# Optimization experiments

Measured on AMD Instinct MI355X. Metric: run time of the kernel, lower is better.

The kernel has to match this reference:

```python
import jax, jax.numpy as jnp
import numpy as np

N = 100000      # nodes
E = 3200000     # edges (avg degree 32)
IN_CH = 32
EDGE_DIM = 11
HID = IN_CH + 4 + EDGE_DIM   # 47
OUT = 128


def setup_inputs() -> dict:
    key = jax.random.key(0)
    ks = jax.random.split(key, 10)
    x = jax.random.normal(ks[0], (N, IN_CH), dtype=jnp.float32)
    pos = jax.random.normal(ks[1], (N, 3), dtype=jnp.float32) * 10.0
    nrm = jax.random.normal(ks[2], (N, 3), dtype=jnp.float32)
    normal = nrm / jnp.linalg.norm(nrm, axis=1, keepdims=True)
    # edges with src != dst (avoids degenerate zero-distance point pairs)
    src = jax.random.randint(ks[3], (E,), 0, N)
    off = jax.random.randint(ks[4], (E,), 1, N)
    dst = (src + off) % N
    edge_index = jnp.stack([src, dst], axis=0).astype(jnp.int64)
    edge_attr = jax.random.normal(ks[5], (E, EDGE_DIM), dtype=jnp.float32)
    W1 = jax.random.normal(ks[6], (HID, HID), dtype=jnp.float32) / np.sqrt(HID)
    b1 = jnp.zeros((HID,), dtype=jnp.float32)
    g1 = jnp.ones((HID,), dtype=jnp.float32)
    be1 = jnp.zeros((HID,), dtype=jnp.float32)
    W2 = jax.random.normal(ks[7], (HID, OUT), dtype=jnp.float32) / np.sqrt(HID)
    b2 = jnp.zeros((OUT,), dtype=jnp.float32)
    g2 = jnp.ones((OUT,), dtype=jnp.float32)
    be2 = jnp.zeros((OUT,), dtype=jnp.float32)
    return {"x": x, "pos": pos, "normal": normal, "edge_attr": edge_attr,
            "W1": W1, "b1": b1, "g1": g1, "be1": be1,
            "W2": W2, "b2": b2, "g2": g2, "be2": be2,
            "edge_index": edge_index}


def _angle(v1, v2):
    return jnp.arctan2(jnp.linalg.norm(jnp.cross(v1, v2), axis=1),
                       jnp.sum(v1 * v2, axis=1))


def _layernorm(h, g, b, eps=1e-5):
    mu = jnp.mean(h, axis=-1, keepdims=True)
    var = jnp.var(h, axis=-1, keepdims=True)  # biased, matches torch LayerNorm
    return (h - mu) / jnp.sqrt(var + eps) * g + b


def reference(x, pos, normal, edge_attr, W1, b1, g1, be1, W2, b2, g2, be2, edge_index):
    src, dst = edge_index[0], edge_index[1]  # message flows src(j) -> dst(i)
    pos_i, pos_j = pos[dst], pos[src]
    n_i, n_j = normal[dst], normal[src]
    x_j = x[src]
    pseudo = pos_j - pos_i                                  # [E,3]
    ppf = jnp.stack([jnp.linalg.norm(pseudo, axis=1),
                     _angle(n_i, pseudo),
                     _angle(n_j, pseudo),
                     _angle(n_i, n_j)], axis=1)             # [E,4]
    msg = jnp.concatenate([x_j, ppf, edge_attr], axis=1)    # [E,47]
    # local_nn = MLP([47,47,128]): (Lin->ReLU->LayerNorm->Dropout(eval)) x2
    h = _layernorm(jax.nn.relu(msg @ W1 + b1), g1, be1)     # [E,47]
    h = _layernorm(jax.nn.relu(h @ W2 + b2), g2, be2)       # [E,128]
    out = jax.ops.segment_max(h, dst, num_segments=N)       # scatter-max per target node
    return jnp.where(jnp.isfinite(out), out, 0.0)           # nodes w/o edges -> 0
```

## Files before the change

kernel.cpp:

```cpp
#include <hip/hip_runtime.h>
#include <cstdint>
#include <cstddef>


typedef _Float16 f16x8 __attribute__((ext_vector_type(8)));
typedef _Float16 f16x2 __attribute__((ext_vector_type(2)));
typedef float    f32x4 __attribute__((ext_vector_type(4)));

#define ENC_NEGINF 0x007FFFFFu
#define LDK 64
#define LDH 132

__device__ __forceinline__ int swz(int row, int col) {
    return (col & 7) | ((((col >> 3) ^ row) & 7) << 3);
}

__device__ __forceinline__ unsigned fenc(float f) {
    unsigned u = __float_as_uint(f);
    return (u & 0x80000000u) ? ~u : (u | 0x80000000u);
}

__device__ __forceinline__ float fdec(unsigned k) {
    if (k == ENC_NEGINF) return 0.0f;
    unsigned u = (k & 0x80000000u) ? (k ^ 0x80000000u) : ~k;
    return __uint_as_float(u);
}

__device__ __forceinline__ f16x2 pkrtz(float a, float b) {
    auto p = __builtin_amdgcn_cvt_pkrtz(a, b);
    return __builtin_bit_cast(f16x2, p);
}

__global__ void init_out_kernel(unsigned* __restrict__ out, int n4) {
    int i = blockIdx.x * blockDim.x + threadIdx.x;
    if (i < n4)
        ((uint4*)out)[i] = make_uint4(ENC_NEGINF, ENC_NEGINF, ENC_NEGINF, ENC_NEGINF);
}

__global__ void finalize_out_kernel(float* __restrict__ out, int n4) {
    int i = blockIdx.x * blockDim.x + threadIdx.x;
    if (i < n4) {
        uint4 k = ((const uint4*)out)[i];
        float4 r;
        r.x = fdec(k.x); r.y = fdec(k.y); r.z = fdec(k.z); r.w = fdec(k.w);
        ((float4*)out)[i] = r;
    }
}

__global__ void zero_kernel(int* __restrict__ p, int n) {
    int i = blockIdx.x * blockDim.x + threadIdx.x;
    if (i < n) p[i] = 0;
}

__global__ void hist_kernel(const int* __restrict__ dstI, int* __restrict__ counts, int E) {
    int i = blockIdx.x * blockDim.x + threadIdx.x;
    if (i < E) atomicAdd(&counts[dstI[i]], 1);
}

__global__ __launch_bounds__(1024) void scan_blk(const int* __restrict__ in,
                                                 int* __restrict__ outp,
                                                 int* __restrict__ bsums, int N) {
    __shared__ int wsum[16];
    const int tid = threadIdx.x, lane = tid & 63, wid = tid >> 6;
    int i = blockIdx.x * 1024 + tid;
    int v = (i < N) ? in[i] : 0;
    int incl = v;
#pragma unroll
    for (int m = 1; m < 64; m <<= 1) {
        int t = __shfl_up(incl, m, 64);
        if (lane >= m) incl += t;
    }
    if (lane == 63) wsum[wid] = incl;
    __syncthreads();
    int woff = 0;
#pragma unroll
    for (int k = 0; k < 16; ++k) woff += (k < wid) ? wsum[k] : 0;
    if (i < N) outp[i] = woff + incl - v;
    if (tid == 1023 && bsums != nullptr) bsums[blockIdx.x] = woff + incl;
}

__global__ void scatter_kernel(const int* __restrict__ srcI, const int* __restrict__ dstI,
                               int* __restrict__ nextp, const int* __restrict__ bsums,
                               int2* __restrict__ se, int* __restrict__ dst_g, int E) {
    int i = blockIdx.x * blockDim.x + threadIdx.x;
    if (i < E) {
        int d = dstI[i];
        int p = bsums[d >> 10] + atomicAdd(&nextp[d], 1);
        se[p] = make_int2(srcI[i], i);
        dst_g[p] = d;
    }
}

__global__ __launch_bounds__(512, 4) void edge_kernel_csr(
    const float* __restrict__ x,   const float* __restrict__ pos,
    const float* __restrict__ nrm, const float* __restrict__ ea,
    const float* __restrict__ W1,  const float* __restrict__ b1,
    const float* __restrict__ g1,  const float* __restrict__ be1,
    const float* __restrict__ W2,  const float* __restrict__ b2,
    const float* __restrict__ g2,  const float* __restrict__ be2,
    const int2* __restrict__ se,   const int* __restrict__ dst_g,
    unsigned* __restrict__ out, int E, int ntiles, int tilesPerBlock)
{
    __shared__ _Float16 W1t[48][LDK];
    __shared__ _Float16 W2t[128][LDK];
    __shared__ _Float16 msgA[128][LDK];
    __shared__ _Float16 h2w[128][LDH];
    __shared__ int dstL[128];

    const int lane = threadIdx.x & 63;
    const int w    = threadIdx.x >> 6;
    const int c16  = lane & 15;
    const int g    = lane >> 4;
    const int row0 = w * 16;

    for (int i = threadIdx.x; i < 48 * 64; i += 512) {
        int n = i >> 6, k = i & 63;
        W1t[n][swz(n, k)] = (n < 47 && k < 47) ? (_Float16)W1[k * 47 + n] : (_Float16)0.f;
    }
    for (int i = threadIdx.x; i < 128 * 64; i += 512) {
        int n = i >> 6, k = i & 63;
        W2t[n][swz(n, k)] = (k < 47) ? (_Float16)W2[k * 128 + n] : (_Float16)0.f;
    }
    for (int i = threadIdx.x; i < 128 * LDK; i += 512)
        (&msgA[0][0])[i] = (_Float16)0.f;

    float b1v[3], g1v[3], be1v[3];
#pragma unroll
    for (int n = 0; n < 3; ++n) {
        int cc = n * 16 + c16;
        bool vld = cc < 47;
        b1v[n]  = vld ? b1[cc]  : 0.f;
        g1v[n]  = vld ? g1[cc]  : 0.f;
        be1v[n] = vld ? be1[cc] : 0.f;
    }
    float b2v[8];
    f16x2 g2pk[4], be2pk[4];
#pragma unroll
    for (int n = 0; n < 8; ++n) b2v[n] = b2[n * 16 + c16];
#pragma unroll
    for (int h = 0; h < 4; ++h) {
        g2pk[h][0]  = (_Float16)g2[(2 * h) * 16 + c16];
        g2pk[h][1]  = (_Float16)g2[(2 * h + 1) * 16 + c16];
        be2pk[h][0] = (_Float16)be2[(2 * h) * 16 + c16];
        be2pk[h][1] = (_Float16)be2[(2 * h + 1) * 16 + c16];
    }
    __syncthreads();

    const int xr = lane >> 2;
    const int xc = (lane & 3) * 8;
    const int eg = lane / 11, ec = lane - eg * 11;
    const bool ea_act  = lane < 44;
    const bool geo_act = lane < 48;

    const int tbeg = blockIdx.x * tilesPerBlock;
    int tend = tbeg + tilesPerBlock;
    if (tend > ntiles) tend = ntiles;

    for (int tile = tbeg; tile < tend; ++tile) {
        const int base = tile * 128 + row0;

        {
            int p = base + xr;
            bool vx = p < E;
            int s = vx ? se[p].x : 0;
            const float4* xp = (const float4*)(x + (size_t)s * 32 + xc);
            float4 xa = xp[0];
            float4 xb = xp[1];

            float eav0 = 0.f, eav1 = 0.f, eav2 = 0.f, eav3 = 0.f;
            if (ea_act) {
                int p0 = base + 0 * 4 + eg, p1 = base + 1 * 4 + eg;
                int p2 = base + 2 * 4 + eg, p3 = base + 3 * 4 + eg;
                int e0 = (p0 < E) ? se[p0].y : 0;
                int e1 = (p1 < E) ? se[p1].y : 0;
                int e2 = (p2 < E) ? se[p2].y : 0;
                int e3 = (p3 < E) ? se[p3].y : 0;
                eav0 = (p0 < E) ? ea[(size_t)e0 * 11 + ec] : 0.f;
                eav1 = (p1 < E) ? ea[(size_t)e1 * 11 + ec] : 0.f;
                eav2 = (p2 < E) ? ea[(size_t)e2 * 11 + ec] : 0.f;
                eav3 = (p3 < E) ? ea[(size_t)e3 * 11 + ec] : 0.f;
            }

            float gpix = 0.f, gpiy = 0.f, gpiz = 0.f;
            float gpjx = 0.f, gpjy = 0.f, gpjz = 0.f;
            float gnix = 0.f, gniy = 0.f, gniz = 0.f;
            float gnjx = 0.f, gnjy = 0.f, gnjz = 0.f;
            int pd = -1;
            if (geo_act) {
                int pg = base + c16;
                bool v = pg < E;
                int s2 = v ? se[pg].x : 0;
                int d2 = v ? dst_g[pg] : 0;
                pd = v ? d2 : -1;
                gpix = pos[d2 * 3 + 0]; gpiy = pos[d2 * 3 + 1]; gpiz = pos[d2 * 3 + 2];
                gpjx = pos[s2 * 3 + 0]; gpjy = pos[s2 * 3 + 1]; gpjz = pos[s2 * 3 + 2];
                gnix = nrm[d2 * 3 + 0]; gniy = nrm[d2 * 3 + 1]; gniz = nrm[d2 * 3 + 2];
                gnjx = nrm[s2 * 3 + 0]; gnjy = nrm[s2 * 3 + 1]; gnjz = nrm[s2 * 3 + 2];
            }

            {
                int r = row0 + xr;
                f16x8 hv;
                hv[0] = (_Float16)(vx ? xa.x : 0.f); hv[1] = (_Float16)(vx ? xa.y : 0.f);
                hv[2] = (_Float16)(vx ? xa.z : 0.f); hv[3] = (_Float16)(vx ? xa.w : 0.f);
                hv[4] = (_Float16)(vx ? xb.x : 0.f); hv[5] = (_Float16)(vx ? xb.y : 0.f);
                hv[6] = (_Float16)(vx ? xb.z : 0.f); hv[7] = (_Float16)(vx ? xb.w : 0.f);
                *(f16x8*)&msgA[r][swz(r, xc)] = hv;
            }
            if (ea_act) {
                int r0 = row0 + 0 * 4 + eg; msgA[r0][swz(r0, 36 + ec)] = (_Float16)eav0;
                int r1 = row0 + 1 * 4 + eg; msgA[r1][swz(r1, 36 + ec)] = (_Float16)eav1;
                int r2 = row0 + 2 * 4 + eg; msgA[r2][swz(r2, 36 + ec)] = (_Float16)eav2;
                int r3 = row0 + 3 * 4 + eg; msgA[r3][swz(r3, 36 + ec)] = (_Float16)eav3;
            }
            if (geo_act) {
                int r = row0 + c16;
                float px = gpjx - gpix, py = gpjy - gpiy, pz = gpjz - gpiz;
                float v1x, v1y, v1z, v2x, v2y, v2z;
                if (g == 0)      { v1x = gnix; v1y = gniy; v1z = gniz; v2x = px;   v2y = py;   v2z = pz; }
                else if (g == 1) { v1x = gnjx; v1y = gnjy; v1z = gnjz; v2x = px;   v2y = py;   v2z = pz; }
                else             { v1x = gnix; v1y = gniy; v1z = gniz; v2x = gnjx; v2y = gnjy; v2z = gnjz; }
                float cx = v1y * v2z - v1z * v2y;
                float cy = v1z * v2x - v1x * v2z;
                float cz = v1x * v2y - v1y * v2x;
                float ang = atan2f(sqrtf(cx * cx + cy * cy + cz * cz),
                                   v1x * v2x + v1y * v2y + v1z * v2z);
                msgA[r][swz(r, 33 + g)] = (_Float16)ang;
                if (g == 0) {
                    msgA[r][swz(r, 32)] = (_Float16)sqrtf(px * px + py * py + pz * pz);
                    dstL[r] = pd;
                }
            }
        }

        f32x4 acc1[3];
#pragma unroll
        for (int n = 0; n < 3; ++n) acc1[n] = (f32x4){0.f, 0.f, 0.f, 0.f};
#pragma unroll
        for (int ks = 0; ks < 2; ++ks) {
            int ar = row0 + c16;
            f16x8 a = *(const f16x8*)&msgA[ar][swz(ar, ks * 32 + g * 8)];
#pragma unroll
            for (int n = 0; n < 3; ++n) {
                int br = n * 16 + c16;
                f16x8 b = *(const f16x8*)&W1t[br][swz(br, ks * 32 + g * 8)];
                acc1[n] = __builtin_amdgcn_mfma_f32_16x16x32_f16(a, b, acc1[n], 0, 0, 0);
            }
        }
#pragma unroll
        for (int q = 0; q < 4; ++q) {
            float t0 = fmaxf(acc1[0][q] + b1v[0], 0.f);
            float t1 = fmaxf(acc1[1][q] + b1v[1], 0.f);
            float t2 = fmaxf(acc1[2][q] + b1v[2], 0.f);
            float s = t0 + t1 + t2;
            float s2 = t0 * t0 + t1 * t1 + t2 * t2;
#pragma unroll
            for (int m = 1; m < 16; m <<= 1) {
                s  += __shfl_xor(s,  m, 64);
                s2 += __shfl_xor(s2, m, 64);
            }
            float mu  = s * (1.f / 47.f);
            float var = s2 * (1.f / 47.f) - mu * mu;
            float rs  = rsqrtf(var + 1e-5f);
            int r = row0 + 4 * g + q;
            msgA[r][swz(r, c16)]      = (_Float16)((t0 - mu) * rs * g1v[0] + be1v[0]);
            msgA[r][swz(r, 16 + c16)] = (_Float16)((t1 - mu) * rs * g1v[1] + be1v[1]);
            msgA[r][swz(r, 32 + c16)] = (_Float16)((t2 - mu) * rs * g1v[2] + be1v[2]);
        }

        f32x4 acc2[8];
#pragma unroll
        for (int n = 0; n < 8; ++n) acc2[n] = (f32x4){0.f, 0.f, 0.f, 0.f};
#pragma unroll
        for (int ks = 0; ks < 2; ++ks) {
            int ar = row0 + c16;
            f16x8 a = *(const f16x8*)&msgA[ar][swz(ar, ks * 32 + g * 8)];
#pragma unroll
            for (int n = 0; n < 8; ++n) {
                int br = n * 16 + c16;
                f16x8 b = *(const f16x8*)&W2t[br][swz(br, ks * 32 + g * 8)];
                acc2[n] = __builtin_amdgcn_mfma_f32_16x16x32_f16(a, b, acc2[n], 0, 0, 0);
            }
        }
#pragma unroll
        for (int q = 0; q < 4; ++q) {
            float t[8];
            float s = 0.f, s2 = 0.f;
#pragma unroll
            for (int n = 0; n < 8; ++n) {
                t[n] = fmaxf(acc2[n][q] + b2v[n], 0.f);
                s += t[n]; s2 += t[n] * t[n];
            }
#pragma unroll
            for (int m = 1; m < 16; m <<= 1) {
                s  += __shfl_xor(s,  m, 64);
                s2 += __shfl_xor(s2, m, 64);
            }
            float mu  = s * (1.f / 128.f);
            float var = s2 * (1.f / 128.f) - mu * mu;
            float rs  = rsqrtf(var + 1e-5f);
            int r = row0 + 4 * g + q;
            f16x2 apk = pkrtz(rs, rs);
            f16x2 cpk = pkrtz(-mu * rs, -mu * rs);
#pragma unroll
            for (int h = 0; h < 4; ++h) {
                f16x2 tpk = pkrtz(t[2 * h], t[2 * h + 1]);
                f16x2 z   = tpk * apk + cpk;
                f16x2 hvp = z * g2pk[h] + be2pk[h];
                h2w[r][(2 * h) * 16 + c16]     = hvp[0];
                h2w[r][(2 * h + 1) * 16 + c16] = hvp[1];
            }
        }

        {
            f16x2 mneg; mneg[0] = mneg[1] = (_Float16)(-65504.f);
            f16x2 mx = mneg;
            int segStart = 0;
            int dcur = dstL[row0];
#pragma unroll
            for (int r = 0; r < 16; ++r) {
                f16x2 pk = *(const f16x2*)&h2w[row0 + r][lane * 2];
                mx[0] = (pk[0] > mx[0]) ? pk[0] : mx[0];
                mx[1] = (pk[1] > mx[1]) ? pk[1] : mx[1];
                int dnext = (r < 15) ? dstL[row0 + r + 1] : -2;
                if (dnext != dcur) {
                    if (dcur >= 0) {
                        unsigned e0 = fenc((float)mx[0]);
                        unsigned e1 = fenc((float)mx[1]);
                        unsigned* orow = out + (size_t)dcur * 128 + lane * 2;
                        if (segStart > 0 && r < 15) {
                            unsigned long long pk2 =
                                ((unsigned long long)e1 << 32) | (unsigned long long)e0;
                            *(unsigned long long*)orow = pk2;
                        } else {
                            atomicMax(orow,     e0);
                            atomicMax(orow + 1, e1);
                        }
                    }
                    mx = mneg;
                    segStart = r + 1; dcur = dnext;
                }
            }
        }
    }
}

#define LDKF 72
__global__ __launch_bounds__(256) void edge_kernel_atomic(
    const float* __restrict__ x,   const float* __restrict__ pos,
    const float* __restrict__ nrm, const float* __restrict__ ea,
    const float* __restrict__ W1,  const float* __restrict__ b1,
    const float* __restrict__ g1,  const float* __restrict__ be1,
    const float* __restrict__ W2,  const float* __restrict__ b2,
    const float* __restrict__ g2,  const float* __restrict__ be2,
    const int* __restrict__ srcI,  const int* __restrict__ dstI,
    unsigned* __restrict__ out, int E, int ntiles)
{
    __shared__ _Float16 W1t[48][LDKF];
    __shared__ _Float16 W2t[128][LDKF];
    __shared__ _Float16 msgA[64][LDKF];
    __shared__ int dst_s[64];

    const int lane = threadIdx.x & 63;
    const int w    = threadIdx.x >> 6;
    const int c16  = lane & 15;
    const int g    = lane >> 4;

    for (int i = threadIdx.x; i < 48 * 64; i += 256) {
        int n = i >> 6, k = i & 63;
        W1t[n][k] = (n < 47 && k < 47) ? (_Float16)W1[k * 47 + n] : (_Float16)0.f;
    }
    for (int i = threadIdx.x; i < 128 * 64; i += 256) {
        int n = i >> 6, k = i & 63;
        W2t[n][k] = (k < 47) ? (_Float16)W2[k * 128 + n] : (_Float16)0.f;
    }
    for (int i = threadIdx.x; i < 64 * LDKF; i += 256)
        (&msgA[0][0])[i] = (_Float16)0.f;

    float b1v[3], g1v[3], be1v[3];
#pragma unroll
    for (int n = 0; n < 3; ++n) {
        int cc = n * 16 + c16;
        bool vld = cc < 47;
        b1v[n]  = vld ? b1[cc]  : 0.f;
        g1v[n]  = vld ? g1[cc]  : 0.f;
        be1v[n] = vld ? be1[cc] : 0.f;
    }
    float b2v[8], g2v[8], be2v[8];
#pragma unroll
    for (int n = 0; n < 8; ++n) {
        int cc = n * 16 + c16;
        b2v[n] = b2[cc]; g2v[n] = g2[cc]; be2v[n] = be2[cc];
    }
    __syncthreads();

    for (int tile = blockIdx.x; tile < ntiles; tile += gridDim.x) {
        const int base = tile * 64 + w * 16;
        const int row0 = w * 16;
#pragma unroll
        for (int i = 0; i < 8; ++i) {
            int el = i * 2 + (lane >> 5);
            int e  = base + el;
            int c  = lane & 31;
            float v = 0.f;
            if (e < E) v = x[(size_t)srcI[e] * 32 + c];
            msgA[row0 + el][c] = (_Float16)v;
        }
        if (lane < 44) {
            int eg = lane / 11, c = lane - eg * 11;
#pragma unroll
            for (int i = 0; i < 4; ++i) {
                int el = i * 4 + eg;
                int e  = base + el;
                float v = 0.f;
                if (e < E) v = ea[(size_t)e * 11 + c];
                msgA[row0 + el][36 + c] = (_Float16)v;
            }
        }
        if (lane < 48) {
            int el = c16;
            int e  = base + el;
            int s = 0, d = 0;
            bool vld = e < E;
            if (vld) { s = srcI[e]; d = dstI[e]; }
            float pix = pos[d * 3 + 0], piy = pos[d * 3 + 1], piz = pos[d * 3 + 2];
            float pjx = pos[s * 3 + 0], pjy = pos[s * 3 + 1], pjz = pos[s * 3 + 2];
            float nix = nrm[d * 3 + 0], niy = nrm[d * 3 + 1], niz = nrm[d * 3 + 2];
            float njx = nrm[s * 3 + 0], njy = nrm[s * 3 + 1], njz = nrm[s * 3 + 2];
            float px = pjx - pix, py = pjy - piy, pz = pjz - piz;
            float v1x, v1y, v1z, v2x, v2y, v2z;
            if (g == 0)      { v1x = nix; v1y = niy; v1z = niz; v2x = px;  v2y = py;  v2z = pz;  }
            else if (g == 1) { v1x = njx; v1y = njy; v1z = njz; v2x = px;  v2y = py;  v2z = pz;  }
            else             { v1x = nix; v1y = niy; v1z = niz; v2x = njx; v2y = njy; v2z = njz; }
            float cx = v1y * v2z - v1z * v2y;
            float cy = v1z * v2x - v1x * v2z;
            float cz = v1x * v2y - v1y * v2x;
            float ang = atan2f(sqrtf(cx * cx + cy * cy + cz * cz),
                               v1x * v2x + v1y * v2y + v1z * v2z);
            msgA[row0 + el][33 + g] = (_Float16)ang;
            if (g == 0) {
                msgA[row0 + el][32] = (_Float16)sqrtf(px * px + py * py + pz * pz);
                dst_s[row0 + el] = vld ? d : -1;
            }
        }

        f32x4 acc1[3];
#pragma unroll
        for (int n = 0; n < 3; ++n) acc1[n] = (f32x4){0.f, 0.f, 0.f, 0.f};
#pragma unroll
        for (int ks = 0; ks < 2; ++ks) {
            f16x8 a = *(const f16x8*)&msgA[row0 + c16][ks * 32 + g * 8];
#pragma unroll
            for (int n = 0; n < 3; ++n) {
                f16x8 b = *(const f16x8*)&W1t[n * 16 + c16][ks * 32 + g * 8];
                acc1[n] = __builtin_amdgcn_mfma_f32_16x16x32_f16(a, b, acc1[n], 0, 0, 0);
            }
        }
#pragma unroll
        for (int q = 0; q < 4; ++q) {
            float t0 = fmaxf(acc1[0][q] + b1v[0], 0.f);
            float t1 = fmaxf(acc1[1][q] + b1v[1], 0.f);
            float t2 = fmaxf(acc1[2][q] + b1v[2], 0.f);
            float s = t0 + t1 + t2;
            float s2 = t0 * t0 + t1 * t1 + t2 * t2;
#pragma unroll
            for (int m = 1; m < 16; m <<= 1) {
                s  += __shfl_xor(s,  m, 64);
                s2 += __shfl_xor(s2, m, 64);
            }
            float mu  = s * (1.f / 47.f);
            float var = s2 * (1.f / 47.f) - mu * mu;
            float rs  = rsqrtf(var + 1e-5f);
            int r = row0 + 4 * g + q;
            msgA[r][c16]      = (_Float16)((t0 - mu) * rs * g1v[0] + be1v[0]);
            msgA[r][16 + c16] = (_Float16)((t1 - mu) * rs * g1v[1] + be1v[1]);
            msgA[r][32 + c16] = (_Float16)((t2 - mu) * rs * g1v[2] + be1v[2]);
        }

        f32x4 acc2[8];
#pragma unroll
        for (int n = 0; n < 8; ++n) acc2[n] = (f32x4){0.f, 0.f, 0.f, 0.f};
#pragma unroll
        for (int ks = 0; ks < 2; ++ks) {
            f16x8 a = *(const f16x8*)&msgA[row0 + c16][ks * 32 + g * 8];
#pragma unroll
            for (int n = 0; n < 8; ++n) {
                f16x8 b = *(const f16x8*)&W2t[n * 16 + c16][ks * 32 + g * 8];
                acc2[n] = __builtin_amdgcn_mfma_f32_16x16x32_f16(a, b, acc2[n], 0, 0, 0);
            }
        }
        int4 dd = *(const int4*)&dst_s[row0 + 4 * g];
#pragma unroll
        for (int q = 0; q < 4; ++q) {
            float t[8];
            float s = 0.f, s2 = 0.f;
#pragma unroll
            for (int n = 0; n < 8; ++n) {
                t[n] = fmaxf(acc2[n][q] + b2v[n], 0.f);
                s += t[n]; s2 += t[n] * t[n];
            }
#pragma unroll
            for (int m = 1; m < 16; m <<= 1) {
                s  += __shfl_xor(s,  m, 64);
                s2 += __shfl_xor(s2, m, 64);
            }
            float mu  = s * (1.f / 128.f);
            float var = s2 * (1.f / 128.f) - mu * mu;
            float rs  = rsqrtf(var + 1e-5f);
            int d = (&dd.x)[q];
            if (d >= 0) {
                unsigned* orow = out + (size_t)d * 128u;
#pragma unroll
                for (int n = 0; n < 8; ++n) {
                    float o = (t[n] - mu) * rs * g2v[n] + be2v[n];
                    atomicMax(orow + n * 16 + c16, fenc(o));
                }
            }
        }
    }
}

extern "C" void kernel_launch(void* const* d_in, const int* in_sizes, int n_in,
                              void* d_out, int out_size, void* d_ws, size_t ws_size,
                              hipStream_t stream) {
    const float* x   = (const float*)d_in[0];
    const float* pos = (const float*)d_in[1];
    const float* nrm = (const float*)d_in[2];
    const float* ea  = (const float*)d_in[3];
    const float* W1  = (const float*)d_in[4];
    const float* b1  = (const float*)d_in[5];
    const float* g1  = (const float*)d_in[6];
    const float* be1 = (const float*)d_in[7];
    const float* W2  = (const float*)d_in[8];
    const float* b2  = (const float*)d_in[9];
    const float* g2  = (const float*)d_in[10];
    const float* be2 = (const float*)d_in[11];
    const int*   idx = (const int*)d_in[12];

    const int N = in_sizes[0] / 32;
    const int E = in_sizes[3] / 11;
    const int* srcI = idx;
    const int* dstI = idx + E;

    unsigned* outU = (unsigned*)d_out;
    const int n = N * 128;

    init_out_kernel<<<(n / 4 + 255) / 256, 256, 0, stream>>>(outU, n / 4);

    const int nb = (N + 1023) / 1024;
    const size_t needed = (size_t)E * 8 + (size_t)(2LL * N + E + nb) * 4;

    if (ws_size >= needed) {
        int2* se     = (int2*)d_ws;
        int*  counts = (int*)(se + E);
        int*  nextp  = counts + N;
        int*  dst_g  = nextp + N;
        int*  bsums  = dst_g + E;

        zero_kernel<<<(N + 255) / 256, 256, 0, stream>>>(counts, N);
        hist_kernel<<<(E + 255) / 256, 256, 0, stream>>>(dstI, counts, E);
        scan_blk<<<nb, 1024, 0, stream>>>(counts, nextp, bsums, N);
        scan_blk<<<1, 1024, 0, stream>>>(bsums, bsums, (int*)nullptr, nb);
        scatter_kernel<<<(E + 255) / 256, 256, 0, stream>>>(srcI, dstI, nextp, bsums,
                                                            se, dst_g, E);

        const int ntiles = (E + 127) / 128;
        int grid = ntiles < 512 ? ntiles : 512;
        int tpb  = (ntiles + grid - 1) / grid;
        edge_kernel_csr<<<grid, 512, 0, stream>>>(x, pos, nrm, ea,
                                                  W1, b1, g1, be1,
                                                  W2, b2, g2, be2,
                                                  se, dst_g,
                                                  outU, E, ntiles, tpb);
    } else {
        const int ntiles = (E + 63) / 64;
        int grid = ntiles < 4096 ? ntiles : 4096;
        edge_kernel_atomic<<<grid, 256, 0, stream>>>(x, pos, nrm, ea,
                                                     W1, b1, g1, be1,
                                                     W2, b2, g2, be2,
                                                     srcI, dstI, outU, E, ntiles);
    }

    finalize_out_kernel<<<(n / 4 + 255) / 256, 256, 0, stream>>>((float*)d_out, n / 4);
}
```

Measured before the change: 852.8 us.

## Software-prefetch next tile's edge indices and edge attributes across loop iterations

In the main edge loop, the sorted edge indices (src, edge id, dst) for the next tile are loaded into registers one iteration ahead. The edge-attribute gathers for the next tile are issued between layer 1 and layer 2. This hides the dependent index-then-gather latency behind the MLP compute. It also swaps the zeroing kernel for hipMemsetAsync. The cost is higher register pressure, which may lower occupancy.

Measured after the change: 842.3 us. Within noise of the previous version (-1.2%).

```diff
diff --git a/kernel.cpp b/kernel.cpp
--- a/kernel.cpp
+++ b/kernel.cpp
@@ -45,11 +45,6 @@
         r.x = fdec(k.x); r.y = fdec(k.y); r.z = fdec(k.z); r.w = fdec(k.w);
         ((float4*)out)[i] = r;
     }
-}
-
-__global__ void zero_kernel(int* __restrict__ p, int n) {
-    int i = blockIdx.x * blockDim.x + threadIdx.x;
-    if (i < n) p[i] = 0;
 }
 
 __global__ void hist_kernel(const int* __restrict__ dstI, int* __restrict__ counts, int E) {
@@ -155,47 +150,81 @@
     const int tbeg = blockIdx.x * tilesPerBlock;
     int tend = tbeg + tilesPerBlock;
     if (tend > ntiles) tend = ntiles;
+    if (tbeg >= tend) return;
+
+    int   pf_sx = 0;
+    int   pf_e0 = -1, pf_e1 = -1, pf_e2 = -1, pf_e3 = -1;
+    int   pf_gs = 0,  pf_gd = -1;
+    float pf_ea0 = 0.f, pf_ea1 = 0.f, pf_ea2 = 0.f, pf_ea3 = 0.f;
+
+    {
+        const int b2 = tbeg * 128 + row0;
+        int p = b2 + xr;
+        pf_sx = (p < E) ? se[p].x : 0;
+        if (ea_act) {
+            int p0 = b2 + eg, p1 = b2 + 4 + eg, p2 = b2 + 8 + eg, p3 = b2 + 12 + eg;
+            pf_e0 = (p0 < E) ? se[p0].y : -1;
+            pf_e1 = (p1 < E) ? se[p1].y : -1;
+            pf_e2 = (p2 < E) ? se[p2].y : -1;
+            pf_e3 = (p3 < E) ? se[p3].y : -1;
+            pf_ea0 = (pf_e0 >= 0) ? ea[(size_t)pf_e0 * 11 + ec] : 0.f;
+            pf_ea1 = (pf_e1 >= 0) ? ea[(size_t)pf_e1 * 11 + ec] : 0.f;
+            pf_ea2 = (pf_e2 >= 0) ? ea[(size_t)pf_e2 * 11 + ec] : 0.f;
+            pf_ea3 = (pf_e3 >= 0) ? ea[(size_t)pf_e3 * 11 + ec] : 0.f;
+        }
+        if (geo_act) {
+            int pg = b2 + c16;
+            bool v = pg < E;
+            pf_gs = v ? se[pg].x : 0;
+            pf_gd = v ? dst_g[pg] : -1;
+        }
+    }
 
     for (int tile = tbeg; tile < tend; ++tile) {
         const int base = tile * 128 + row0;
+        const bool more = (tile + 1 < tend);
+
+        const int   c_sx  = pf_sx;
+        const int   c_gs  = pf_gs;
+        const int   c_gd  = pf_gd;
+        const float cea0 = pf_ea0, cea1 = pf_ea1, cea2 = pf_ea2, cea3 = pf_ea3;
+
+        if (more) {
+            const int b2 = base + 128;
+            int p = b2 + xr;
+            pf_sx = (p < E) ? se[p].x : 0;
+            if (ea_act) {
+                int p0 = b2 + eg, p1 = b2 + 4 + eg, p2 = b2 + 8 + eg, p3 = b2 + 12 + eg;
+                pf_e0 = (p0 < E) ? se[p0].y : -1;
+                pf_e1 = (p1 < E) ? se[p1].y : -1;
+                pf_e2 = (p2 < E) ? se[p2].y : -1;
+                pf_e3 = (p3 < E) ? se[p3].y : -1;
+            }
+            if (geo_act) {
+                int pg = b2 + c16;
+                bool v = pg < E;
+                pf_gs = v ? se[pg].x : 0;
+                pf_gd = v ? dst_g[pg] : -1;
+            }
+        }
 
         {
             int p = base + xr;
             bool vx = p < E;
-            int s = vx ? se[p].x : 0;
-            const float4* xp = (const float4*)(x + (size_t)s * 32 + xc);
+            const float4* xp = (const float4*)(x + (size_t)c_sx * 32 + xc);
             float4 xa = xp[0];
             float4 xb = xp[1];
-
-            float eav0 = 0.f, eav1 = 0.f, eav2 = 0.f, eav3 = 0.f;
-            if (ea_act) {
-                int p0 = base + 0 * 4 + eg, p1 = base + 1 * 4 + eg;
-                int p2 = base + 2 * 4 + eg, p3 = base + 3 * 4 + eg;
-                int e0 = (p0 < E) ? se[p0].y : 0;
-                int e1 = (p1 < E) ? se[p1].y : 0;
-                int e2 = (p2 < E) ? se[p2].y : 0;
-                int e3 = (p3 < E) ? se[p3].y : 0;
-                eav0 = (p0 < E) ? ea[(size_t)e0 * 11 + ec] : 0.f;
-                eav1 = (p1 < E) ? ea[(size_t)e1 * 11 + ec] : 0.f;
-                eav2 = (p2 < E) ? ea[(size_t)e2 * 11 + ec] : 0.f;
-                eav3 = (p3 < E) ? ea[(size_t)e3 * 11 + ec] : 0.f;
-            }
 
             float gpix = 0.f, gpiy = 0.f, gpiz = 0.f;
             float gpjx = 0.f, gpjy = 0.f, gpjz = 0.f;
             float gnix = 0.f, gniy = 0.f, gniz = 0.f;
             float gnjx = 0.f, gnjy = 0.f, gnjz = 0.f;
-            int pd = -1;
             if (geo_act) {
-                int pg = base + c16;
-                bool v = pg < E;
-                int s2 = v ? se[pg].x : 0;
-                int d2 = v ? dst_g[pg] : 0;
-                pd = v ? d2 : -1;
+                int d2 = (c_gd < 0) ? 0 : c_gd;
                 gpix = pos[d2 * 3 + 0]; gpiy = pos[d2 * 3 + 1]; gpiz = pos[d2 * 3 + 2];
-                gpjx = pos[s2 * 3 + 0]; gpjy = pos[s2 * 3 + 1]; gpjz = pos[s2 * 3 + 2];
+                gpjx = pos[c_gs * 3 + 0]; gpjy = pos[c_gs * 3 + 1]; gpjz = pos[c_gs * 3 + 2];
                 gnix = nrm[d2 * 3 + 0]; gniy = nrm[d2 * 3 + 1]; gniz = nrm[d2 * 3 + 2];
-                gnjx = nrm[s2 * 3 + 0]; gnjy = nrm[s2 * 3 + 1]; gnjz = nrm[s2 * 3 + 2];
+                gnjx = nrm[c_gs * 3 + 0]; gnjy = nrm[c_gs * 3 + 1]; gnjz = nrm[c_gs * 3 + 2];
             }
 
             {
@@ -208,10 +237,10 @@
                 *(f16x8*)&msgA[r][swz(r, xc)] = hv;
             }
             if (ea_act) {
-                int r0 = row0 + 0 * 4 + eg; msgA[r0][swz(r0, 36 + ec)] = (_Float16)eav0;
-                int r1 = row0 + 1 * 4 + eg; msgA[r1][swz(r1, 36 + ec)] = (_Float16)eav1;
-                int r2 = row0 + 2 * 4 + eg; msgA[r2][swz(r2, 36 + ec)] = (_Float16)eav2;
-                int r3 = row0 + 3 * 4 + eg; msgA[r3][swz(r3, 36 + ec)] = (_Float16)eav3;
+                int r0 = row0 + 0 * 4 + eg; msgA[r0][swz(r0, 36 + ec)] = (_Float16)cea0;
+                int r1 = row0 + 1 * 4 + eg; msgA[r1][swz(r1, 36 + ec)] = (_Float16)cea1;
+                int r2 = row0 + 2 * 4 + eg; msgA[r2][swz(r2, 36 + ec)] = (_Float16)cea2;
+                int r3 = row0 + 3 * 4 + eg; msgA[r3][swz(r3, 36 + ec)] = (_Float16)cea3;
             }
             if (geo_act) {
                 int r = row0 + c16;
@@ -228,7 +257,7 @@
                 msgA[r][swz(r, 33 + g)] = (_Float16)ang;
                 if (g == 0) {
                     msgA[r][swz(r, 32)] = (_Float16)sqrtf(px * px + py * py + pz * pz);
-                    dstL[r] = pd;
+                    dstL[r] = c_gd;
                 }
             }
         }
@@ -266,6 +295,13 @@
             msgA[r][swz(r, c16)]      = (_Float16)((t0 - mu) * rs * g1v[0] + be1v[0]);
             msgA[r][swz(r, 16 + c16)] = (_Float16)((t1 - mu) * rs * g1v[1] + be1v[1]);
             msgA[r][swz(r, 32 + c16)] = (_Float16)((t2 - mu) * rs * g1v[2] + be1v[2]);
+        }
+
+        if (more && ea_act) {
+            pf_ea0 = (pf_e0 >= 0) ? ea[(size_t)pf_e0 * 11 + ec] : 0.f;
+            pf_ea1 = (pf_e1 >= 0) ? ea[(size_t)pf_e1 * 11 + ec] : 0.f;
+            pf_ea2 = (pf_e2 >= 0) ? ea[(size_t)pf_e2 * 11 + ec] : 0.f;
+            pf_ea3 = (pf_e3 >= 0) ? ea[(size_t)pf_e3 * 11 + ec] : 0.f;
         }
 
         f32x4 acc2[8];
@@ -557,7 +593,7 @@
         int*  dst_g  = nextp + N;
         int*  bsums  = dst_g + E;
 
-        zero_kernel<<<(N + 255) / 256, 256, 0, stream>>>(counts, N);
+        hipMemsetAsync(counts, 0, (size_t)N * 4, stream);
         hist_kernel<<<(E + 255) / 256, 256, 0, stream>>>(dstI, counts, E);
         scan_blk<<<nb, 1024, 0, stream>>>(counts, nextp, bsums, N);
         scan_blk<<<1, 1024, 0, stream>>>(bsums, bsums, (int*)nullptr, nb);
```
